# Performance work log

Measured on AMD Instinct MI355X. Metric: run time of the kernel, lower is better.

Reference implementation:

```python
import jax, jax.numpy as jnp
import numpy as np


def setup_inputs() -> dict:
    key = jax.random.key(0)
    ks = jax.random.split(key, 18)
    B, L, D, E, V = 64, 4096, 512, 256, 32000
    s = 0.05
    return {
        "featureGrid": jax.random.normal(ks[0], (B, L, D), jnp.float32),
        "y_prev": jax.random.uniform(ks[1], (B, V), jnp.float32),
        "out_prev": jax.random.normal(ks[2], (B, D), jnp.float32),
        "h_prev": jax.random.normal(ks[3], (B, D), jnp.float32),
        "c_prev": jax.random.normal(ks[4], (B, D), jnp.float32),
        "embedding": jax.random.normal(ks[5], (V, E), jnp.float32) * s,
        "W_f": jax.random.normal(ks[6], (D + E, D), jnp.float32) * s,
        "W_i": jax.random.normal(ks[7], (D + E, D), jnp.float32) * s,
        "W_g": jax.random.normal(ks[8], (D + E, D), jnp.float32) * s,
        "W_o": jax.random.normal(ks[9], (D + E, D), jnp.float32) * s,
        "b_f": jax.random.normal(ks[10], (D,), jnp.float32) * s,
        "b_i": jax.random.normal(ks[11], (D,), jnp.float32) * s,
        "b_g": jax.random.normal(ks[12], (D,), jnp.float32) * s,
        "b_o": jax.random.normal(ks[13], (D,), jnp.float32) * s,
        "W_e": jax.random.normal(ks[14], (D, D), jnp.float32) * s,
        "W_out": jax.random.normal(ks[15], (2 * D, D), jnp.float32) * s,
        "W_y": jax.random.normal(ks[16], (D, V), jnp.float32) * s,
    }


def reference(featureGrid, y_prev, out_prev, h_prev, c_prev, embedding,
              W_f, W_i, W_g, W_o, b_f, b_i, b_g, b_o, W_e, W_out, W_y):
    # free_run: previous output distribution -> argmax token -> embedding
    tok = jnp.argmax(y_prev, axis=-1)              # [B]
    emb = embedding[tok]                            # [B, E]
    x = jnp.concatenate([emb, out_prev], axis=-1)   # [B, E+D]
    f = jax.nn.sigmoid(x @ W_f + b_f)
    i = jax.nn.sigmoid(x @ W_i + b_i)
    g = jnp.tanh(x @ W_g + b_g)
    o = jax.nn.sigmoid(x @ W_o + b_o)
    c = c_prev * f + i * g                          # [B, D]
    h = jnp.tanh(c) * o                             # [B, D]
    b = h @ W_e                                     # [B, D]
    e = jnp.einsum('bld,bd->bl', featureGrid, b)    # attention scores [B, L]
    a = jax.nn.softmax(e, axis=-1)                  # [B, L]
    z = jnp.einsum('bl,bld->bd', a, featureGrid)    # context [B, D]
    hz = jnp.concatenate([h, z], axis=-1)           # [B, 2D]
    out = jnp.tanh(hz @ W_out)                      # [B, D]
    y = jax.nn.softmax(out @ W_y, axis=-1)          # [B, V]
    return (y, out, h, c)
```

## Files before the change

### kernel.cpp

```cpp
#include <hip/hip_runtime.h>
#include <math.h>

#define NB 64
#define NL 4096
#define ND 512
#define NE 256
#define NV 32000
#define NX 768
#define CHUNKS 32
#define RPC (NL / CHUNKS)
#define RPW (RPC / 4)
#define NV4 (NV / 4)

#define GK_KS 4
#define GK_KL 192
#define WE_KS 4
#define WE_KL 128
#define WO_KS 4
#define WO_KL 256

__global__ void k_argmax(const float* __restrict__ y_prev, int* __restrict__ tok) {
    int b = blockIdx.x, tid = threadIdx.x, lane = tid & 63, wave = tid >> 6;
    const float4* row = (const float4*)(y_prev + (size_t)b * NV);
    float best = -INFINITY; int bi = 0x7fffffff;
    for (int v4 = tid; v4 < NV4; v4 += 1024) {
        float4 x = row[v4];
        int base = v4 * 4;
        if (x.x > best) { best = x.x; bi = base; }
        if (x.y > best) { best = x.y; bi = base + 1; }
        if (x.z > best) { best = x.z; bi = base + 2; }
        if (x.w > best) { best = x.w; bi = base + 3; }
    }
    #pragma unroll
    for (int off = 32; off > 0; off >>= 1) {
        float ob = __shfl_xor(best, off, 64);
        int   oi = __shfl_xor(bi, off, 64);
        if (ob > best || (ob == best && oi < bi)) { best = ob; bi = oi; }
    }
    __shared__ float sv[16]; __shared__ int si[16];
    if (lane == 0) { sv[wave] = best; si[wave] = bi; }
    __syncthreads();
    if (tid == 0) {
        float bb = sv[0]; int ii = si[0];
        for (int w = 1; w < 16; ++w)
            if (sv[w] > bb || (sv[w] == bb && si[w] < ii)) { bb = sv[w]; ii = si[w]; }
        tok[b] = ii;
    }
}

__global__ void k_gates(const float* __restrict__ embedding, const float* __restrict__ out_prev,
                        const int* __restrict__ tok,
                        const float* __restrict__ W_f, const float* __restrict__ W_i,
                        const float* __restrict__ W_g, const float* __restrict__ W_o,
                        float* __restrict__ gp) {
    __shared__ float xs[16][GK_KL];
    int tid = threadIdx.x;
    int cc = blockIdx.x, bg = blockIdx.y, ks = blockIdx.z;
    int k0 = ks * GK_KL;
    for (int e = tid; e < 16 * GK_KL; e += 256) {
        int bi = e / GK_KL, kk = e - bi * GK_KL;
        int b = bg * 16 + bi, k = k0 + kk;
        xs[bi][kk] = (k < NE) ? embedding[(size_t)tok[b] * NE + k]
                              : out_prev[(size_t)b * ND + (k - NE)];
    }
    __syncthreads();
    int ct = tid & 63, bs = tid >> 6;
    int gate = cc >> 1;
    int d = (cc & 1) * 256 + ct * 4;
    const float* W = (gate == 0) ? W_f : (gate == 1) ? W_i : (gate == 2) ? W_g : W_o;
    const float4* Wp = (const float4*)(W + (size_t)k0 * ND + d);
    float acc[4][4] = {};
    #pragma unroll 4
    for (int kk = 0; kk < GK_KL; ++kk) {
        float4 w4 = Wp[kk * (ND / 4)];
        #pragma unroll
        for (int i = 0; i < 4; ++i) {
            float xv = xs[bs * 4 + i][kk];
            acc[i][0] += xv * w4.x; acc[i][1] += xv * w4.y;
            acc[i][2] += xv * w4.z; acc[i][3] += xv * w4.w;
        }
    }
    #pragma unroll
    for (int i = 0; i < 4; ++i) {
        int b = bg * 16 + bs * 4 + i;
        float4 st = make_float4(acc[i][0], acc[i][1], acc[i][2], acc[i][3]);
        *(float4*)&gp[(((size_t)ks * 4 + gate) * NB + b) * ND + d] = st;
    }
}

__global__ void k_lstm(const float* __restrict__ gp, const float* __restrict__ c_prev,
                       const float* __restrict__ b_f, const float* __restrict__ b_i,
                       const float* __restrict__ b_g, const float* __restrict__ b_o,
                       float* __restrict__ h_out, float* __restrict__ c_out) {
    int idx = blockIdx.x * 256 + threadIdx.x;
    int b = idx >> 9, d = idx & 511;
    float F = b_f[d], I = b_i[d], G = b_g[d], O = b_o[d];
    #pragma unroll
    for (int ks = 0; ks < GK_KS; ++ks) {
        F += gp[(((size_t)ks * 4 + 0) * NB + b) * ND + d];
        I += gp[(((size_t)ks * 4 + 1) * NB + b) * ND + d];
        G += gp[(((size_t)ks * 4 + 2) * NB + b) * ND + d];
        O += gp[(((size_t)ks * 4 + 3) * NB + b) * ND + d];
    }
    float f = 1.f / (1.f + __expf(-F));
    float i = 1.f / (1.f + __expf(-I));
    float g = tanhf(G);
    float o = 1.f / (1.f + __expf(-O));
    float c = c_prev[idx] * f + i * g;
    float h = tanhf(c) * o;
    h_out[idx] = h;
    c_out[idx] = c;
}

__global__ void k_we(const float* __restrict__ h, const float* __restrict__ W_e,
                     float* __restrict__ wp) {
    __shared__ float hs[16][WE_KL];
    int tid = threadIdx.x;
    int cc = blockIdx.x, bg = blockIdx.y, ks = blockIdx.z;
    int k0 = ks * WE_KL;
    for (int e = tid; e < 16 * WE_KL; e += 256) {
        int bi = e >> 7, kk = e & 127;
        hs[bi][kk] = h[(size_t)(bg * 16 + bi) * ND + k0 + kk];
    }
    __syncthreads();
    int ct = tid & 63, bs = tid >> 6;
    int col = cc * 256 + ct * 4;
    const float4* Wp = (const float4*)(W_e + (size_t)k0 * ND + col);
    float acc[4][4] = {};
    #pragma unroll 4
    for (int kk = 0; kk < WE_KL; ++kk) {
        float4 w4 = Wp[kk * (ND / 4)];
        #pragma unroll
        for (int i = 0; i < 4; ++i) {
            float xv = hs[bs * 4 + i][kk];
            acc[i][0] += xv * w4.x; acc[i][1] += xv * w4.y;
            acc[i][2] += xv * w4.z; acc[i][3] += xv * w4.w;
        }
    }
    #pragma unroll
    for (int i = 0; i < 4; ++i) {
        int b = bg * 16 + bs * 4 + i;
        float4 st = make_float4(acc[i][0], acc[i][1], acc[i][2], acc[i][3]);
        *(float4*)&wp[((size_t)ks * NB + b) * ND + col] = st;
    }
}

__global__ void k_attn(const float* __restrict__ fg, const float* __restrict__ wp,
                       float* __restrict__ partM, float* __restrict__ partS,
                       float* __restrict__ partZ) {
    int blk = blockIdx.x;
    int b = blk / CHUNKS, chunk = blk - b * CHUNKS;
    int tid = threadIdx.x, wave = tid >> 6, lane = tid & 63;
    float4 bs0 = make_float4(0.f, 0.f, 0.f, 0.f), bs1 = bs0;
    #pragma unroll
    for (int ks = 0; ks < WE_KS; ++ks) {
        const float4* p = (const float4*)(wp + ((size_t)ks * NB + b) * ND + lane * 8);
        float4 a = p[0], c = p[1];
        bs0.x += a.x; bs0.y += a.y; bs0.z += a.z; bs0.w += a.w;
        bs1.x += c.x; bs1.y += c.y; bs1.z += c.z; bs1.w += c.w;
    }
    const float* rowp = fg + ((size_t)b * NL + (size_t)chunk * RPC + wave * RPW) * ND + lane * 8;
    float m = -INFINITY, s = 0.f;
    float z0 = 0, z1 = 0, z2 = 0, z3 = 0, z4 = 0, z5 = 0, z6 = 0, z7 = 0;
    float4 c0v = ((const float4*)rowp)[0];
    float4 c1v = ((const float4*)rowp)[1];
    float4 n0v = ((const float4*)(rowp + ND))[0];
    float4 n1v = ((const float4*)(rowp + ND))[1];
    #pragma unroll 2
    for (int r = 0; r < RPW; ++r) {
        float4 v0 = c0v, v1 = c1v;
        c0v = n0v; c1v = n1v;
        if (r + 2 < RPW) {
            const float* np = rowp + 2 * ND;
            n0v = ((const float4*)np)[0];
            n1v = ((const float4*)np)[1];
        }
        float e = v0.x * bs0.x + v0.y * bs0.y + v0.z * bs0.z + v0.w * bs0.w
                + v1.x * bs1.x + v1.y * bs1.y + v1.z * bs1.z + v1.w * bs1.w;
        #pragma unroll
        for (int off = 32; off > 0; off >>= 1) e += __shfl_xor(e, off, 64);
        if (e > m) {
            float sc = __expf(m - e);
            s *= sc;
            z0 *= sc; z1 *= sc; z2 *= sc; z3 *= sc;
            z4 *= sc; z5 *= sc; z6 *= sc; z7 *= sc;
            m = e;
        }
        float w = __expf(e - m);
        s += w;
        z0 += w * v0.x; z1 += w * v0.y; z2 += w * v0.z; z3 += w * v0.w;
        z4 += w * v1.x; z5 += w * v1.y; z6 += w * v1.z; z7 += w * v1.w;
        rowp += ND;
    }
    __shared__ float wm[4], wsum[4], wz[4][ND];
    float* zp = &wz[wave][lane * 8];
    zp[0] = z0; zp[1] = z1; zp[2] = z2; zp[3] = z3; zp[4] = z4; zp[5] = z5; zp[6] = z6; zp[7] = z7;
    if (lane == 0) { wm[wave] = m; wsum[wave] = s; }
    __syncthreads();
    float M = fmaxf(fmaxf(wm[0], wm[1]), fmaxf(wm[2], wm[3]));
    float e0 = __expf(wm[0] - M), e1 = __expf(wm[1] - M), e2 = __expf(wm[2] - M), e3 = __expf(wm[3] - M);
    if (tid == 0) {
        partM[blk] = M;
        partS[blk] = wsum[0] * e0 + wsum[1] * e1 + wsum[2] * e2 + wsum[3] * e3;
    }
    for (int d = tid; d < ND; d += 256)
        partZ[(size_t)blk * ND + d] = wz[0][d] * e0 + wz[1][d] * e1 + wz[2][d] * e2 + wz[3][d] * e3;
}

__global__ void k_zcomb(const float* __restrict__ partM, const float* __restrict__ partS,
                        const float* __restrict__ partZ, float* __restrict__ z) {
    int b = blockIdx.x, tid = threadIdx.x;
    float M = -INFINITY;
    #pragma unroll
    for (int j = 0; j < CHUNKS; ++j) M = fmaxf(M, partM[b * CHUNKS + j]);
    float w[CHUNKS]; float S = 0.f;
    #pragma unroll
    for (int j = 0; j < CHUNKS; ++j) { w[j] = __expf(partM[b * CHUNKS + j] - M); S += partS[b * CHUNKS + j] * w[j]; }
    float inv = 1.f / S;
    for (int d = tid; d < ND; d += 256) {
        float acc = 0.f;
        #pragma unroll
        for (int j = 0; j < CHUNKS; ++j) acc += w[j] * partZ[((size_t)b * CHUNKS + j) * ND + d];
        z[(size_t)b * ND + d] = acc * inv;
    }
}

__global__ void k_wout(const float* __restrict__ h, const float* __restrict__ z,
                       const float* __restrict__ W_out, float* __restrict__ op) {
    __shared__ float hzs[16][WO_KL];
    int tid = threadIdx.x;
    int cc = blockIdx.x, bg = blockIdx.y, ks = blockIdx.z;
    int k0 = ks * WO_KL;
    for (int e = tid; e < 16 * WO_KL; e += 256) {
        int bi = e >> 8, kk = e & 255;
        int b = bg * 16 + bi, k = k0 + kk;
        hzs[bi][kk] = (k < ND) ? h[(size_t)b * ND + k] : z[(size_t)b * ND + (k - ND)];
    }
    __syncthreads();
    int ct = tid & 63, bs = tid >> 6;
    int col = cc * 256 + ct * 4;
    const float4* Wp = (const float4*)(W_out + (size_t)k0 * ND + col);
    float acc[4][4] = {};
    #pragma unroll 4
    for (int kk = 0; kk < WO_KL; ++kk) {
        float4 w4 = Wp[kk * (ND / 4)];
        #pragma unroll
        for (int i = 0; i < 4; ++i) {
            float xv = hzs[bs * 4 + i][kk];
            acc[i][0] += xv * w4.x; acc[i][1] += xv * w4.y;
            acc[i][2] += xv * w4.z; acc[i][3] += xv * w4.w;
        }
    }
    #pragma unroll
    for (int i = 0; i < 4; ++i) {
        int b = bg * 16 + bs * 4 + i;
        float4 st = make_float4(acc[i][0], acc[i][1], acc[i][2], acc[i][3]);
        *(float4*)&op[((size_t)ks * NB + b) * ND + col] = st;
    }
}

__global__ void k_outfin(const float* __restrict__ op,
                         float* __restrict__ out_f32, float* __restrict__ outT) {
    int idx = blockIdx.x * 512 + threadIdx.x;
    int b = idx >> 9, d = idx & 511;
    float s = 0.f;
    #pragma unroll
    for (int ks = 0; ks < WO_KS; ++ks) s += op[((size_t)ks * NB + b) * ND + d];
    float t = tanhf(s);
    out_f32[idx] = t;
    outT[(size_t)d * NB + b] = t;
}

#define WLOAD(P, G0)                                                          \
    { _Pragma("unroll")                                                       \
      for (int u = 0; u < 8; ++u)                                             \
          P[u] = *(const float4*)(wbase + (size_t)((G0) * 8 + u) * NV); }

#define WCOMP(P, G0)                                                          \
    { _Pragma("unroll")                                                       \
      for (int u = 0; u < 8; ++u) {                                           \
          int dd = ((G0) & 7) * 8 + u;                                        \
          float4 ov = *(const float4*)&os[dd][bq * 4];                        \
          const float ob[4] = {ov.x, ov.y, ov.z, ov.w};                       \
          const float wj[4] = {P[u].x, P[u].y, P[u].z, P[u].w};               \
          _Pragma("unroll")                                                   \
          for (int i = 0; i < 4; ++i) {                                       \
              _Pragma("unroll")                                               \
              for (int j = 0; j < 4; ++j) acc[i][j] += ob[i] * wj[j];         \
          }                                                                   \
      } }

__global__ __launch_bounds__(512, 1) void k_logits(const float* __restrict__ outT,
                                                   const float* __restrict__ W_y,
                                                   float* __restrict__ ylog) {
    __shared__ float os[64][64];
    int tid = threadIdx.x;
    int cg = tid & 31;
    int bq = tid >> 5;
    int c0 = blockIdx.x * 128;
    const float* wbase = W_y + c0 + cg * 4;
    float acc[4][4];
    #pragma unroll
    for (int i = 0; i < 4; ++i)
        #pragma unroll
        for (int j = 0; j < 4; ++j) acc[i][j] = 0.f;
    float4 pA[8], pB[8];
    WLOAD(pA, 0);
    for (int G = 0; G < 64; G += 2) {
        if ((G & 7) == 0) {
            __syncthreads();
            int dt = G >> 3;
            for (int e = tid; e < 4096; e += 512) {
                int dd = e >> 6, bb = e & 63;
                os[dd][bb] = outT[(size_t)(dt * 64 + dd) * NB + bb];
            }
            __syncthreads();
        }
        WLOAD(pB, G + 1);
        WCOMP(pA, G);
        if (G + 2 < 64) WLOAD(pA, G + 2);
        WCOMP(pB, G + 1);
    }
    #pragma unroll
    for (int i = 0; i < 4; ++i) {
        float4 st = make_float4(acc[i][0], acc[i][1], acc[i][2], acc[i][3]);
        *(float4*)&ylog[(size_t)(bq * 4 + i) * NV + c0 + cg * 4] = st;
    }
}

__global__ void k_softmax(float* __restrict__ y) {
    int b = blockIdx.x, tid = threadIdx.x, lane = tid & 63, wave = tid >> 6;
    float4* row = (float4*)(y + (size_t)b * NV);
    float4 r[8];
    int cnt = 0;
    for (int v4 = tid; v4 < NV4; v4 += 1024) r[cnt++] = row[v4];
    float m = -INFINITY;
    for (int k = 0; k < cnt; ++k)
        m = fmaxf(m, fmaxf(fmaxf(r[k].x, r[k].y), fmaxf(r[k].z, r[k].w)));
    #pragma unroll
    for (int off = 32; off > 0; off >>= 1) m = fmaxf(m, __shfl_xor(m, off, 64));
    __shared__ float red[16];
    __shared__ float bcast[2];
    if (lane == 0) red[wave] = m;
    __syncthreads();
    if (tid == 0) {
        float M = red[0];
        for (int w = 1; w < 16; ++w) M = fmaxf(M, red[w]);
        bcast[0] = M;
    }
    __syncthreads();
    float M = bcast[0];
    float s = 0.f;
    for (int k = 0; k < cnt; ++k) {
        r[k].x = __expf(r[k].x - M); r[k].y = __expf(r[k].y - M);
        r[k].z = __expf(r[k].z - M); r[k].w = __expf(r[k].w - M);
        s += r[k].x + r[k].y + r[k].z + r[k].w;
    }
    #pragma unroll
    for (int off = 32; off > 0; off >>= 1) s += __shfl_xor(s, off, 64);
    if (lane == 0) red[wave] = s;
    __syncthreads();
    if (tid == 0) {
        float S = 0.f;
        for (int w = 0; w < 16; ++w) S += red[w];
        bcast[1] = 1.f / S;
    }
    __syncthreads();
    float inv = bcast[1];
    cnt = 0;
    for (int v4 = tid; v4 < NV4; v4 += 1024) {
        float4 e4 = r[cnt++];
        e4.x *= inv; e4.y *= inv; e4.z *= inv; e4.w *= inv;
        row[v4] = e4;
    }
}

extern "C" void kernel_launch(void* const* d_in, const int* in_sizes, int n_in,
                              void* d_out, int out_size, void* d_ws, size_t ws_size,
                              hipStream_t stream) {
    (void)in_sizes; (void)n_in; (void)out_size; (void)ws_size;
    const float* featureGrid = (const float*)d_in[0];
    const float* y_prev      = (const float*)d_in[1];
    const float* out_prev    = (const float*)d_in[2];
    const float* c_prev      = (const float*)d_in[4];
    const float* embedding   = (const float*)d_in[5];
    const float* W_f = (const float*)d_in[6];
    const float* W_i = (const float*)d_in[7];
    const float* W_g = (const float*)d_in[8];
    const float* W_o = (const float*)d_in[9];
    const float* b_f = (const float*)d_in[10];
    const float* b_i = (const float*)d_in[11];
    const float* b_g = (const float*)d_in[12];
    const float* b_o = (const float*)d_in[13];
    const float* W_e   = (const float*)d_in[14];
    const float* W_out = (const float*)d_in[15];
    const float* W_y   = (const float*)d_in[16];

    float* y_f32   = (float*)d_out;
    float* out_f32 = y_f32 + (size_t)NB * NV;
    float* h_f32   = out_f32 + (size_t)NB * ND;
    float* c_f32   = h_f32 + (size_t)NB * ND;

    float* ws = (float*)d_ws;
    int*   tok   = (int*)ws;
    float* gp    = ws + 64;
    float* wp    = gp + (size_t)GK_KS * 4 * NB * ND;
    float* zctx  = wp + (size_t)WE_KS * NB * ND;
    float* partM = zctx + NB * ND;
    float* partS = partM + NB * CHUNKS;
    float* partZ = partS + NB * CHUNKS;
    float* op    = partZ + (size_t)NB * CHUNKS * ND;
    float* outT  = op + (size_t)WO_KS * NB * ND;

    k_argmax<<<NB, 1024, 0, stream>>>(y_prev, tok);
    k_gates<<<dim3(8, 4, GK_KS), 256, 0, stream>>>(embedding, out_prev, tok, W_f, W_i, W_g, W_o, gp);
    k_lstm<<<128, 256, 0, stream>>>(gp, c_prev, b_f, b_i, b_g, b_o, h_f32, c_f32);
    k_we<<<dim3(2, 4, WE_KS), 256, 0, stream>>>(h_f32, W_e, wp);
    k_attn<<<NB * CHUNKS, 256, 0, stream>>>(featureGrid, wp, partM, partS, partZ);
    k_zcomb<<<NB, 256, 0, stream>>>(partM, partS, partZ, zctx);
    k_wout<<<dim3(2, 4, WO_KS), 256, 0, stream>>>(h_f32, zctx, W_out, op);
    k_outfin<<<64, 512, 0, stream>>>(op, out_f32, outT);
    k_logits<<<250, 512, 0, stream>>>(outT, W_y, y_f32);
    k_softmax<<<NB, 1024, 0, stream>>>(y_f32);
}
```

Baseline: 302.4 us.

## Fuse split-K reduction and tanh into logits and softmax; remap attn lane loads

Drops the k_outfin kernel. k_wout now writes its split-K partials transposed, and both the logits tile loader and the softmax kernel sum the four partials and apply tanh themselves. In k_attn, each lane now reads two float4 values 256 floats apart instead of eight contiguous floats, so neighbouring lanes issue contiguous 16-byte accesses. The cost is that the tanh and partial sums are recomputed in every logits block, and k_wout's stores become scattered scalar writes.

```diff
diff --git a/kernel.cpp b/kernel.cpp
--- a/kernel.cpp
+++ b/kernel.cpp
@@ -151,29 +151,31 @@
     int blk = blockIdx.x;
     int b = blk / CHUNKS, chunk = blk - b * CHUNKS;
     int tid = threadIdx.x, wave = tid >> 6, lane = tid & 63;
+    int lo4 = lane * 4;
     float4 bs0 = make_float4(0.f, 0.f, 0.f, 0.f), bs1 = bs0;
     #pragma unroll
     for (int ks = 0; ks < WE_KS; ++ks) {
-        const float4* p = (const float4*)(wp + ((size_t)ks * NB + b) * ND + lane * 8);
-        float4 a = p[0], c = p[1];
+        const float* p = wp + ((size_t)ks * NB + b) * ND;
+        float4 a = *(const float4*)(p + lo4);
+        float4 c = *(const float4*)(p + 256 + lo4);
         bs0.x += a.x; bs0.y += a.y; bs0.z += a.z; bs0.w += a.w;
         bs1.x += c.x; bs1.y += c.y; bs1.z += c.z; bs1.w += c.w;
     }
-    const float* rowp = fg + ((size_t)b * NL + (size_t)chunk * RPC + wave * RPW) * ND + lane * 8;
+    const float* rowp = fg + ((size_t)b * NL + (size_t)chunk * RPC + wave * RPW) * ND;
     float m = -INFINITY, s = 0.f;
     float z0 = 0, z1 = 0, z2 = 0, z3 = 0, z4 = 0, z5 = 0, z6 = 0, z7 = 0;
-    float4 c0v = ((const float4*)rowp)[0];
-    float4 c1v = ((const float4*)rowp)[1];
-    float4 n0v = ((const float4*)(rowp + ND))[0];
-    float4 n1v = ((const float4*)(rowp + ND))[1];
+    float4 c0v = *(const float4*)(rowp + lo4);
+    float4 c1v = *(const float4*)(rowp + 256 + lo4);
+    float4 n0v = *(const float4*)(rowp + ND + lo4);
+    float4 n1v = *(const float4*)(rowp + ND + 256 + lo4);
     #pragma unroll 2
     for (int r = 0; r < RPW; ++r) {
         float4 v0 = c0v, v1 = c1v;
         c0v = n0v; c1v = n1v;
         if (r + 2 < RPW) {
             const float* np = rowp + 2 * ND;
-            n0v = ((const float4*)np)[0];
-            n1v = ((const float4*)np)[1];
+            n0v = *(const float4*)(np + lo4);
+            n1v = *(const float4*)(np + 256 + lo4);
         }
         float e = v0.x * bs0.x + v0.y * bs0.y + v0.z * bs0.z + v0.w * bs0.w
                 + v1.x * bs1.x + v1.y * bs1.y + v1.z * bs1.z + v1.w * bs1.w;
@@ -193,8 +195,9 @@
         rowp += ND;
     }
     __shared__ float wm[4], wsum[4], wz[4][ND];
-    float* zp = &wz[wave][lane * 8];
-    zp[0] = z0; zp[1] = z1; zp[2] = z2; zp[3] = z3; zp[4] = z4; zp[5] = z5; zp[6] = z6; zp[7] = z7;
+    float* zp = &wz[wave][0];
+    zp[lo4 + 0] = z0; zp[lo4 + 1] = z1; zp[lo4 + 2] = z2; zp[lo4 + 3] = z3;
+    zp[256 + lo4 + 0] = z4; zp[256 + lo4 + 1] = z5; zp[256 + lo4 + 2] = z6; zp[256 + lo4 + 3] = z7;
     if (lane == 0) { wm[wave] = m; wsum[wave] = s; }
     __syncthreads();
     float M = fmaxf(fmaxf(wm[0], wm[1]), fmaxf(wm[2], wm[3]));
@@ -226,7 +229,7 @@
 }
 
 __global__ void k_wout(const float* __restrict__ h, const float* __restrict__ z,
-                       const float* __restrict__ W_out, float* __restrict__ op) {
+                       const float* __restrict__ W_out, float* __restrict__ opT) {
     __shared__ float hzs[16][WO_KL];
     int tid = threadIdx.x;
     int cc = blockIdx.x, bg = blockIdx.y, ks = blockIdx.z;
@@ -254,21 +257,10 @@
     #pragma unroll
     for (int i = 0; i < 4; ++i) {
         int b = bg * 16 + bs * 4 + i;
-        float4 st = make_float4(acc[i][0], acc[i][1], acc[i][2], acc[i][3]);
-        *(float4*)&op[((size_t)ks * NB + b) * ND + col] = st;
-    }
-}
-
-__global__ void k_outfin(const float* __restrict__ op,
-                         float* __restrict__ out_f32, float* __restrict__ outT) {
-    int idx = blockIdx.x * 512 + threadIdx.x;
-    int b = idx >> 9, d = idx & 511;
-    float s = 0.f;
-    #pragma unroll
-    for (int ks = 0; ks < WO_KS; ++ks) s += op[((size_t)ks * NB + b) * ND + d];
-    float t = tanhf(s);
-    out_f32[idx] = t;
-    outT[(size_t)d * NB + b] = t;
+        #pragma unroll
+        for (int j = 0; j < 4; ++j)
+            opT[((size_t)ks * ND + col + j) * NB + b] = acc[i][j];
+    }
 }
 
 #define WLOAD(P, G0)                                                          \
@@ -290,7 +282,7 @@
           }                                                                   \
       } }
 
-__global__ __launch_bounds__(512, 1) void k_logits(const float* __restrict__ outT,
+__global__ __launch_bounds__(512, 1) void k_logits(const float* __restrict__ opT,
                                                    const float* __restrict__ W_y,
                                                    float* __restrict__ ylog) {
     __shared__ float os[64][64];
@@ -312,7 +304,12 @@
             int dt = G >> 3;
             for (int e = tid; e < 4096; e += 512) {
                 int dd = e >> 6, bb = e & 63;
-                os[dd][bb] = outT[(size_t)(dt * 64 + dd) * NB + bb];
+                size_t base = (size_t)(dt * 64 + dd) * NB + bb;
+                float sm = opT[(size_t)0 * ND * NB + base]
+                         + opT[(size_t)1 * ND * NB + base]
+                         + opT[(size_t)2 * ND * NB + base]
+                         + opT[(size_t)3 * ND * NB + base];
+                os[dd][bb] = tanhf(sm);
             }
             __syncthreads();
         }
@@ -328,8 +325,16 @@
     }
 }
 
-__global__ void k_softmax(float* __restrict__ y) {
+__global__ void k_softmax(const float* __restrict__ opT, float* __restrict__ out_f32,
+                          float* __restrict__ y) {
     int b = blockIdx.x, tid = threadIdx.x, lane = tid & 63, wave = tid >> 6;
+    if (tid < 512) {
+        float sm = opT[((size_t)0 * ND + tid) * NB + b]
+                 + opT[((size_t)1 * ND + tid) * NB + b]
+                 + opT[((size_t)2 * ND + tid) * NB + b]
+                 + opT[((size_t)3 * ND + tid) * NB + b];
+        out_f32[(size_t)b * ND + tid] = tanhf(sm);
+    }
     float4* row = (float4*)(y + (size_t)b * NV);
     float4 r[8];
     int cnt = 0;
@@ -409,8 +414,7 @@
     float* partM = zctx + NB * ND;
     float* partS = partM + NB * CHUNKS;
     float* partZ = partS + NB * CHUNKS;
-    float* op    = partZ + (size_t)NB * CHUNKS * ND;
-    float* outT  = op + (size_t)WO_KS * NB * ND;
+    float* opT   = partZ + (size_t)NB * CHUNKS * ND;
 
     k_argmax<<<NB, 1024, 0, stream>>>(y_prev, tok);
     k_gates<<<dim3(8, 4, GK_KS), 256, 0, stream>>>(embedding, out_prev, tok, W_f, W_i, W_g, W_o, gp);
@@ -418,8 +422,7 @@
     k_we<<<dim3(2, 4, WE_KS), 256, 0, stream>>>(h_f32, W_e, wp);
     k_attn<<<NB * CHUNKS, 256, 0, stream>>>(featureGrid, wp, partM, partS, partZ);
     k_zcomb<<<NB, 256, 0, stream>>>(partM, partS, partZ, zctx);
-    k_wout<<<dim3(2, 4, WO_KS), 256, 0, stream>>>(h_f32, zctx, W_out, op);
-    k_outfin<<<64, 512, 0, stream>>>(op, out_f32, outT);
-    k_logits<<<250, 512, 0, stream>>>(outT, W_y, y_f32);
-    k_softmax<<<NB, 1024, 0, stream>>>(y_f32);
-}
+    k_wout<<<dim3(2, 4, WO_KS), 256, 0, stream>>>(h_f32, zctx, W_out, opT);
+    k_logits<<<250, 512, 0, stream>>>(opT, W_y, y_f32);
+    k_softmax<<<NB, 1024, 0, stream>>>(opT, out_f32, y_f32);
+}
```

Measured after the change: 328.4 us. 8.6% more time.
